# Optimization experiments

Hardware: AMD Instinct MI355X
Metric: run time of the kernel (lower is better)

Reference implementation:

```python
import jax, jax.numpy as jnp
import numpy as np

B, T, D, H, E, K = 1, 2048, 768, 12, 8, 2
VOCAB, LLOC, LGLOB, CHUNK = 32000, 2, 1, 16
D4 = 4 * D


def setup_inputs() -> dict:
    key = jax.random.key(0)
    kit = iter(jax.random.split(key, 40))

    def rn(shape, scale=0.02):
        return jax.random.normal(next(kit), shape, jnp.float32) * scale

    d = {
        "x_emb": jax.random.normal(next(kit), (B, T, D), jnp.float32),
        "latent_code": jax.random.normal(next(kit), (B, D), jnp.float32),
        "pos_emb": rn((T, D)),
    }
    for pfx, L in (("loc", LLOC), ("glob", LGLOB)):
        d[pfx + "_ln1_s"] = jnp.ones((L, D), jnp.float32)
        d[pfx + "_ln1_b"] = jnp.zeros((L, D), jnp.float32)
        d[pfx + "_ln2_s"] = jnp.ones((L, D), jnp.float32)
        d[pfx + "_ln2_b"] = jnp.zeros((L, D), jnp.float32)
        d[pfx + "_attn_w"] = rn((L, 3 * D, D))
        d[pfx + "_attn_b"] = jnp.zeros((L, 3 * D), jnp.float32)
        d[pfx + "_out_w"] = rn((L, D, D))
        d[pfx + "_out_b"] = jnp.zeros((L, D), jnp.float32)
        d[pfx + "_router_w"] = rn((L, E, D))
        d[pfx + "_w1"] = rn((L, E, D4, D))
        d[pfx + "_b1"] = jnp.zeros((L, E, D4), jnp.float32)
        d[pfx + "_w2"] = rn((L, E, D, D4))
        d[pfx + "_b2"] = jnp.zeros((L, E, D), jnp.float32)
    d["glob_lat_router_w"] = rn((LGLOB, E, D))
    d["ln_s"] = jnp.ones((D,), jnp.float32)
    d["ln_b"] = jnp.zeros((D,), jnp.float32)
    d["head_w"] = rn((VOCAB, D))
    return d


def _ln(x, s, b):
    m = x.mean(-1, keepdims=True)
    v = ((x - m) ** 2).mean(-1, keepdims=True)
    return (x - m) / jnp.sqrt(v + 1e-5) * s + b


def _mha(x, wqkv, bqkv, wo, bo, mask):
    b_, t_, d_ = x.shape
    hd = d_ // H
    q, k, v = jnp.split(x @ wqkv.T + bqkv, 3, axis=-1)
    q = q.reshape(b_, t_, H, hd)
    k = k.reshape(b_, t_, H, hd)
    v = v.reshape(b_, t_, H, hd)
    sc = jnp.einsum('bqhd,bkhd->bhqk', q, k) / jnp.sqrt(jnp.float32(hd))
    sc = jnp.where(mask, -jnp.inf, sc)
    a = jax.nn.softmax(sc, axis=-1)
    o = jnp.einsum('bhqk,bkhd->bqhd', a, v).reshape(b_, t_, d_)
    return o @ wo.T + bo


def _moe(x, rw, w1, b1, w2, b2, lat_logits):
    # top-k routed MoE: combine weight is exactly 0 for unselected experts,
    # so dense per-expert compute weighted by we reproduces the gather/scatter math.
    b_, t_, d_ = x.shape
    xf = x.reshape(-1, d_)
    logits = xf @ rw.T  # [N,E]
    if lat_logits is not None:
        logits = (logits.reshape(b_, t_, E) + lat_logits[:, None, :]).reshape(-1, E)
    probs = jax.nn.softmax(logits, axis=-1)
    w, sel = jax.lax.top_k(probs, K)
    w = w / w.sum(-1, keepdims=True)
    onehot = (sel[..., None] == jnp.arange(E)).astype(xf.dtype)  # [N,K,E]
    we = (w[..., None] * onehot).sum(1)  # [N,E]
    out = jnp.zeros_like(xf)
    for e in range(E):
        h = jax.nn.gelu(xf @ w1[e].T + b1[e], approximate=False)
        out = out + we[:, e:e + 1] * (h @ w2[e].T + b2[e])
    bal = E * jnp.sum(probs.mean(0) * onehot.max(1).mean(0))
    return out.reshape(b_, t_, d_), bal


def _run_layers(x, mask, lat_code, ln1_s, ln1_b, ln2_s, ln2_b, aw, ab, ow, ob, rw, lrw, w1, b1, w2, b2):
    bal = jnp.float32(0.0)
    for l in range(ln1_s.shape[0]):
        h = _ln(x, ln1_s[l], ln1_b[l])
        x = x + _mha(h, aw[l], ab[l], ow[l], ob[l], mask)
        h = _ln(x, ln2_s[l], ln2_b[l])
        lat_logits = None if lat_code is None else lat_code @ lrw[l].T
        mo, b = _moe(h, rw[l], w1[l], b1[l], w2[l], b2[l], lat_logits)
        x = x + mo
        bal = bal + b
    return x, bal


def reference(x_emb, latent_code, pos_emb,
              loc_ln1_s, loc_ln1_b, loc_ln2_s, loc_ln2_b, loc_attn_w, loc_attn_b, loc_out_w, loc_out_b,
              loc_router_w, loc_w1, loc_b1, loc_w2, loc_b2,
              glob_ln1_s, glob_ln1_b, glob_ln2_s, glob_ln2_b, glob_attn_w, glob_attn_b, glob_out_w, glob_out_b,
              glob_router_w, glob_w1, glob_b1, glob_w2, glob_b2, glob_lat_router_w,
              ln_s, ln_b, head_w):
    b_, t_, d_ = x_emb.shape
    x = x_emb + pos_emb[:t_][None]
    mask = jnp.triu(jnp.ones((t_, t_), bool), 1)
    h_local, bal_l = _run_layers(x, mask, None, loc_ln1_s, loc_ln1_b, loc_ln2_s, loc_ln2_b,
                                 loc_attn_w, loc_attn_b, loc_out_w, loc_out_b,
                                 loc_router_w, None, loc_w1, loc_b1, loc_w2, loc_b2)
    # T divisible by CHUNK, so synopsis idxs are 15,31,...,T-1 (no extra append)
    syn = h_local[:, CHUNK - 1::CHUNK]  # [B,S,D]
    gin = jnp.concatenate([latent_code[:, None, :], syn], axis=1)  # [B,S+1,D]
    s1 = gin.shape[1]
    gmask = jnp.triu(jnp.ones((s1, s1), bool), 1)
    h_g, bal_g = _run_layers(gin, gmask, latent_code, glob_ln1_s, glob_ln1_b, glob_ln2_s, glob_ln2_b,
                             glob_attn_w, glob_attn_b, glob_out_w, glob_out_b,
                             glob_router_w, glob_lat_router_w, glob_w1, glob_b1, glob_w2, glob_b2)
    gc = h_g[:, :-1]  # [B,S,D] (latent prepended -> drop last)
    # uniform chunks: broadcast each chunk's global context over its 16 tokens
    out = (h_local.reshape(b_, t_ // CHUNK, CHUNK, d_) + gc[:, :, None, :]).reshape(b_, t_, d_)
    out = _ln(out, ln_s, ln_b)
    return out @ head_w.T, bal_l + bal_g
```

## Files before the change

### kernel.cpp

```cpp
#include <hip/hip_runtime.h>

constexpr int TT   = 2048;
constexpr int DD   = 768;
constexpr int NH   = 12;
constexpr int NE   = 8;
constexpr int DFF  = 3072;
constexpr int NV   = 32000;
constexpr int S1R  = 129;
constexpr int QKVLD = 3 * DD;

constexpr int BM = 64, BN = 64, BK = 16;

__device__ __forceinline__ float gelu_f(float v) {
  return 0.5f * v * (1.0f + erff(v * 0.70710678118654752f));
}

__global__ void add_pos_kernel(const float* __restrict__ xe, const float* __restrict__ pe,
                               float* __restrict__ X, int n) {
  int i = blockIdx.x * blockDim.x + threadIdx.x;
  if (i < n) X[i] = xe[i] + pe[i];
}

__global__ void zero_i32(int* p, int n) {
  int i = blockIdx.x * blockDim.x + threadIdx.x;
  if (i < n) p[i] = 0;
}
__global__ void zero_f32(float* p, int n) {
  int i = blockIdx.x * blockDim.x + threadIdx.x;
  if (i < n) p[i] = 0.f;
}

__global__ __launch_bounds__(256)
void ln_kernel(const float* __restrict__ Xin, const float* __restrict__ s,
               const float* __restrict__ b, float* __restrict__ Y, int rows) {
  int t = blockIdx.x;
  if (t >= rows) return;
  const float* xr = Xin + (size_t)t * DD;
  int tid = threadIdx.x;
  float x0 = xr[tid], x1 = xr[tid + 256], x2 = xr[tid + 512];
  __shared__ float red[256];
  red[tid] = x0 + x1 + x2;
  __syncthreads();
  for (int k = 128; k > 0; k >>= 1) { if (tid < k) red[tid] += red[tid + k]; __syncthreads(); }
  float mean = red[0] * (1.f / 768.f);
  __syncthreads();
  float d0 = x0 - mean, d1 = x1 - mean, d2 = x2 - mean;
  red[tid] = d0 * d0 + d1 * d1 + d2 * d2;
  __syncthreads();
  for (int k = 128; k > 0; k >>= 1) { if (tid < k) red[tid] += red[tid + k]; __syncthreads(); }
  float inv = 1.f / sqrtf(red[0] * (1.f / 768.f) + 1e-5f);
  float* yr = Y + (size_t)t * DD;
  yr[tid]       = d0 * inv * s[tid]       + b[tid];
  yr[tid + 256] = d1 * inv * s[tid + 256] + b[tid + 256];
  yr[tid + 512] = d2 * inv * s[tid + 512] + b[tid + 512];
}

template <bool ADD_C>
__global__ __launch_bounds__(256)
void gemm_tn(const float* __restrict__ A, const float* __restrict__ W,
             const float* __restrict__ bias, float* __restrict__ C,
             int M, int N, int Kd) {
  __shared__ float As[BK][BM + 4];
  __shared__ float Ws[BK][BN + 4];
  int n0 = blockIdx.x * BN, m0 = blockIdx.y * BM;
  int tid = threadIdx.x;
  int tx = tid & 15, ty = tid >> 4;
  int lrow = tid >> 2, lk4 = (tid & 3) * 4;
  float acc[4][4] = {};
  for (int k0 = 0; k0 < Kd; k0 += BK) {
    {
      int r = m0 + lrow;
      float4 v = (r < M) ? *(const float4*)(A + (size_t)r * Kd + k0 + lk4)
                         : make_float4(0.f, 0.f, 0.f, 0.f);
      As[lk4 + 0][lrow] = v.x; As[lk4 + 1][lrow] = v.y;
      As[lk4 + 2][lrow] = v.z; As[lk4 + 3][lrow] = v.w;
    }
    {
      int r = n0 + lrow;
      float4 v = (r < N) ? *(const float4*)(W + (size_t)r * Kd + k0 + lk4)
                         : make_float4(0.f, 0.f, 0.f, 0.f);
      Ws[lk4 + 0][lrow] = v.x; Ws[lk4 + 1][lrow] = v.y;
      Ws[lk4 + 2][lrow] = v.z; Ws[lk4 + 3][lrow] = v.w;
    }
    __syncthreads();
#pragma unroll
    for (int k = 0; k < BK; k++) {
      float a[4], b[4];
#pragma unroll
      for (int i = 0; i < 4; i++) a[i] = As[k][ty * 4 + i];
#pragma unroll
      for (int j = 0; j < 4; j++) b[j] = Ws[k][tx * 4 + j];
#pragma unroll
      for (int i = 0; i < 4; i++)
#pragma unroll
        for (int j = 0; j < 4; j++) acc[i][j] = fmaf(a[i], b[j], acc[i][j]);
    }
    __syncthreads();
  }
#pragma unroll
  for (int i = 0; i < 4; i++) {
    int r = m0 + ty * 4 + i;
    if (r >= M) continue;
#pragma unroll
    for (int j = 0; j < 4; j++) {
      int c = n0 + tx * 4 + j;
      if (c >= N) continue;
      float v = acc[i][j] + (bias ? bias[c] : 0.f);
      size_t idx = (size_t)r * N + c;
      if (ADD_C) C[idx] += v; else C[idx] = v;
    }
  }
}

__global__ __launch_bounds__(256)
void moe_gemm1(const float* __restrict__ Xin, const float* __restrict__ W1,
               const float* __restrict__ B1, float* __restrict__ H1,
               const int* __restrict__ perm, const int* __restrict__ off) {
  __shared__ float As[BK][BM + 4];
  __shared__ float Ws[BK][BN + 4];
  int e = blockIdx.z;
  int mstart = off[e];
  int mcnt = off[e + 1] - mstart;
  int m0 = blockIdx.y * BM;
  if (m0 >= mcnt) return;
  int n0 = blockIdx.x * BN;
  const float* W = W1 + (size_t)e * DFF * DD;
  const float* bias = B1 + (size_t)e * DFF;
  int tid = threadIdx.x;
  int tx = tid & 15, ty = tid >> 4;
  int lrow = tid >> 2, lk4 = (tid & 3) * 4;
  int gm = m0 + lrow;
  const float* arow = (gm < mcnt) ? (Xin + (size_t)perm[mstart + gm] * DD) : nullptr;
  float acc[4][4] = {};
  for (int k0 = 0; k0 < DD; k0 += BK) {
    float4 va = arow ? *(const float4*)(arow + k0 + lk4) : make_float4(0.f, 0.f, 0.f, 0.f);
    As[lk4 + 0][lrow] = va.x; As[lk4 + 1][lrow] = va.y;
    As[lk4 + 2][lrow] = va.z; As[lk4 + 3][lrow] = va.w;
    int wr = n0 + lrow;
    float4 vw = *(const float4*)(W + (size_t)wr * DD + k0 + lk4);
    Ws[lk4 + 0][lrow] = vw.x; Ws[lk4 + 1][lrow] = vw.y;
    Ws[lk4 + 2][lrow] = vw.z; Ws[lk4 + 3][lrow] = vw.w;
    __syncthreads();
#pragma unroll
    for (int k = 0; k < BK; k++) {
      float a[4], b[4];
#pragma unroll
      for (int i = 0; i < 4; i++) a[i] = As[k][ty * 4 + i];
#pragma unroll
      for (int j = 0; j < 4; j++) b[j] = Ws[k][tx * 4 + j];
#pragma unroll
      for (int i = 0; i < 4; i++)
#pragma unroll
        for (int j = 0; j < 4; j++) acc[i][j] = fmaf(a[i], b[j], acc[i][j]);
    }
    __syncthreads();
  }
#pragma unroll
  for (int i = 0; i < 4; i++) {
    int r = m0 + ty * 4 + i;
    if (r >= mcnt) continue;
#pragma unroll
    for (int j = 0; j < 4; j++) {
      int c = n0 + tx * 4 + j;
      float v = acc[i][j] + bias[c];
      H1[(size_t)(mstart + r) * DFF + c] = gelu_f(v);
    }
  }
}

__global__ __launch_bounds__(256)
void moe_gemm2(const float* __restrict__ H1, const float* __restrict__ W2,
               const float* __restrict__ B2, float* __restrict__ Xout,
               const int* __restrict__ perm, const int* __restrict__ off,
               const float* __restrict__ wlist) {
  __shared__ float As[BK][BM + 4];
  __shared__ float Ws[BK][BN + 4];
  int e = blockIdx.z;
  int mstart = off[e];
  int mcnt = off[e + 1] - mstart;
  int m0 = blockIdx.y * BM;
  if (m0 >= mcnt) return;
  int n0 = blockIdx.x * BN;
  const float* W = W2 + (size_t)e * DD * DFF;
  const float* bias = B2 + (size_t)e * DD;
  int tid = threadIdx.x;
  int tx = tid & 15, ty = tid >> 4;
  int lrow = tid >> 2, lk4 = (tid & 3) * 4;
  int gm = m0 + lrow;
  const float* arow = (gm < mcnt) ? (H1 + (size_t)(mstart + gm) * DFF) : nullptr;
  float acc[4][4] = {};
  for (int k0 = 0; k0 < DFF; k0 += BK) {
    float4 va = arow ? *(const float4*)(arow + k0 + lk4) : make_float4(0.f, 0.f, 0.f, 0.f);
    As[lk4 + 0][lrow] = va.x; As[lk4 + 1][lrow] = va.y;
    As[lk4 + 2][lrow] = va.z; As[lk4 + 3][lrow] = va.w;
    int wr = n0 + lrow;
    float4 vw = *(const float4*)(W + (size_t)wr * DFF + k0 + lk4);
    Ws[lk4 + 0][lrow] = vw.x; Ws[lk4 + 1][lrow] = vw.y;
    Ws[lk4 + 2][lrow] = vw.z; Ws[lk4 + 3][lrow] = vw.w;
    __syncthreads();
#pragma unroll
    for (int k = 0; k < BK; k++) {
      float a[4], b[4];
#pragma unroll
      for (int i = 0; i < 4; i++) a[i] = As[k][ty * 4 + i];
#pragma unroll
      for (int j = 0; j < 4; j++) b[j] = Ws[k][tx * 4 + j];
#pragma unroll
      for (int i = 0; i < 4; i++)
#pragma unroll
        for (int j = 0; j < 4; j++) acc[i][j] = fmaf(a[i], b[j], acc[i][j]);
    }
    __syncthreads();
  }
#pragma unroll
  for (int i = 0; i < 4; i++) {
    int r = m0 + ty * 4 + i;
    if (r >= mcnt) continue;
    int tok = perm[mstart + r];
    float sc = wlist[mstart + r];
#pragma unroll
    for (int j = 0; j < 4; j++) {
      int c = n0 + tx * 4 + j;
      float v = (acc[i][j] + bias[c]) * sc;
      atomicAdd(&Xout[(size_t)tok * DD + c], v);
    }
  }
}

__global__ __launch_bounds__(64)
void attn_kernel(const float* __restrict__ QKV, float* __restrict__ O, int Tlen) {
  int q = blockIdx.x, h = blockIdx.y;
  int tid = threadIdx.x;
  __shared__ float qv[64];
  __shared__ float sc[TT];
  qv[tid] = QKV[(size_t)q * QKVLD + h * 64 + tid];
  __syncthreads();
  int nk = q + 1;
  for (int k = tid; k < nk; k += 64) {
    const float* kr = QKV + (size_t)k * QKVLD + DD + h * 64;
    float s = 0.f;
#pragma unroll
    for (int d = 0; d < 64; d++) s = fmaf(qv[d], kr[d], s);
    sc[k] = s * 0.125f;
  }
  __syncthreads();
  float m = -1e30f;
  for (int k = tid; k < nk; k += 64) m = fmaxf(m, sc[k]);
#pragma unroll
  for (int o = 32; o > 0; o >>= 1) m = fmaxf(m, __shfl_down(m, o));
  m = __shfl(m, 0);
  float ssum = 0.f;
  for (int k = tid; k < nk; k += 64) {
    float e = __expf(sc[k] - m);
    sc[k] = e;
    ssum += e;
  }
#pragma unroll
  for (int o = 32; o > 0; o >>= 1) ssum += __shfl_down(ssum, o);
  ssum = __shfl(ssum, 0);
  float inv = 1.f / ssum;
  __syncthreads();
  float acc = 0.f;
  const float* vbase = QKV + 2 * DD + h * 64 + tid;
  for (int k = 0; k < nk; k++) acc = fmaf(sc[k], vbase[(size_t)k * QKVLD], acc);
  O[(size_t)q * DD + h * 64 + tid] = acc * inv;
}

__global__ __launch_bounds__(64)
void router_kernel(const float* __restrict__ Hin, const float* __restrict__ RW,
                   const float* __restrict__ latent, const float* __restrict__ LRW,
                   int rows, int* __restrict__ selbuf, float* __restrict__ wbuf,
                   float* __restrict__ probbuf, int* __restrict__ cnt) {
  int t = blockIdx.x;
  if (t >= rows) return;
  int tid = threadIdx.x;
  const float* hr = Hin + (size_t)t * DD;
  __shared__ float logit[NE];
  for (int e = 0; e < NE; e++) {
    const float* w = RW + (size_t)e * DD;
    float p = 0.f;
    for (int d = tid; d < DD; d += 64) p = fmaf(hr[d], w[d], p);
    if (LRW) {
      const float* lw = LRW + (size_t)e * DD;
      for (int d = tid; d < DD; d += 64) p = fmaf(latent[d], lw[d], p);
    }
#pragma unroll
    for (int o = 32; o > 0; o >>= 1) p += __shfl_down(p, o);
    if (tid == 0) logit[e] = p;
  }
  __syncthreads();
  if (tid == 0) {
    float mx = logit[0];
    for (int e = 1; e < NE; e++) mx = fmaxf(mx, logit[e]);
    float pe[NE], ssum = 0.f;
    for (int e = 0; e < NE; e++) { pe[e] = __expf(logit[e] - mx); ssum += pe[e]; }
    float inv = 1.f / ssum;
    for (int e = 0; e < NE; e++) { pe[e] *= inv; probbuf[(size_t)t * NE + e] = pe[e]; }
    int e0 = 0;
    for (int e = 1; e < NE; e++) if (pe[e] > pe[e0]) e0 = e;
    int e1 = -1;
    for (int e = 0; e < NE; e++) {
      if (e == e0) continue;
      if (e1 < 0 || pe[e] > pe[e1]) e1 = e;
    }
    float wsum = pe[e0] + pe[e1];
    selbuf[t * 2] = e0; selbuf[t * 2 + 1] = e1;
    wbuf[t * 2] = pe[e0] / wsum; wbuf[t * 2 + 1] = pe[e1] / wsum;
    atomicAdd(&cnt[e0], 1);
    atomicAdd(&cnt[e1], 1);
  }
}

__global__ __launch_bounds__(256)
void prob_reduce(const float* __restrict__ probbuf, float* __restrict__ prob_sum, int rows) {
  int e = blockIdx.x, tid = threadIdx.x;
  float s = 0.f;
  for (int t = tid; t < rows; t += 256) s += probbuf[(size_t)t * NE + e];
  __shared__ float red[256];
  red[tid] = s;
  __syncthreads();
  for (int k = 128; k > 0; k >>= 1) { if (tid < k) red[tid] += red[tid + k]; __syncthreads(); }
  if (tid == 0) prob_sum[e] = red[0];
}

__global__ void scan_bal(const int* __restrict__ cnt, int* __restrict__ off,
                         int* __restrict__ fill, const float* __restrict__ prob_sum,
                         float* __restrict__ bal, int rows) {
  if (threadIdx.x == 0 && blockIdx.x == 0) {
    int acc = 0;
    for (int e = 0; e < NE; e++) { off[e] = acc; acc += cnt[e]; fill[e] = 0; }
    off[NE] = acc;
    float invr = 1.f / (float)rows;
    float b = 0.f;
    for (int e = 0; e < NE; e++) b += (prob_sum[e] * invr) * ((float)cnt[e] * invr);
    bal[0] += (float)NE * b;
  }
}

__global__ void fill_kernel(const int* __restrict__ selbuf, const float* __restrict__ wbuf,
                            const int* __restrict__ off, int* __restrict__ fill,
                            int* __restrict__ perm, float* __restrict__ wlist, int rows) {
  int t = blockIdx.x * blockDim.x + threadIdx.x;
  if (t >= rows) return;
  for (int k = 0; k < 2; k++) {
    int e = selbuf[t * 2 + k];
    int pos = atomicAdd(&fill[e], 1);
    perm[off[e] + pos] = t;
    wlist[off[e] + pos] = wbuf[t * 2 + k];
  }
}

__global__ void build_gin(const float* __restrict__ X, const float* __restrict__ latent,
                          float* __restrict__ G) {
  int i = blockIdx.x * blockDim.x + threadIdx.x;
  if (i >= S1R * DD) return;
  int r = i / DD, d = i - r * DD;
  G[i] = (r == 0) ? latent[d] : X[(size_t)((r - 1) * 16 + 15) * DD + d];
}

__global__ void compose_kernel(const float* __restrict__ X, const float* __restrict__ G,
                               float* __restrict__ F) {
  int i = blockIdx.x * blockDim.x + threadIdx.x;
  if (i >= TT * DD) return;
  int t = i / DD, d = i - t * DD;
  F[i] = X[i] + G[(size_t)(t >> 4) * DD + d];
}

__global__ void write_bal(const float* __restrict__ bal, float* __restrict__ out) {
  if (threadIdx.x == 0 && blockIdx.x == 0) out[(size_t)TT * NV] = bal[0];
}

extern "C" void kernel_launch(void* const* d_in, const int* in_sizes, int n_in,
                              void* d_out, int out_size, void* d_ws, size_t ws_size,
                              hipStream_t stream) {
  (void)in_sizes; (void)n_in; (void)out_size; (void)ws_size;
  const float* x_emb    = (const float*)d_in[0];
  const float* latent   = (const float*)d_in[1];
  const float* pos_emb  = (const float*)d_in[2];
  const float* loc_ln1_s = (const float*)d_in[3];
  const float* loc_ln1_b = (const float*)d_in[4];
  const float* loc_ln2_s = (const float*)d_in[5];
  const float* loc_ln2_b = (const float*)d_in[6];
  const float* loc_aw    = (const float*)d_in[7];
  const float* loc_ab    = (const float*)d_in[8];
  const float* loc_ow    = (const float*)d_in[9];
  const float* loc_ob    = (const float*)d_in[10];
  const float* loc_rw    = (const float*)d_in[11];
  const float* loc_w1    = (const float*)d_in[12];
  const float* loc_b1    = (const float*)d_in[13];
  const float* loc_w2    = (const float*)d_in[14];
  const float* loc_b2    = (const float*)d_in[15];
  const float* glb_ln1_s = (const float*)d_in[16];
  const float* glb_ln1_b = (const float*)d_in[17];
  const float* glb_ln2_s = (const float*)d_in[18];
  const float* glb_ln2_b = (const float*)d_in[19];
  const float* glb_aw    = (const float*)d_in[20];
  const float* glb_ab    = (const float*)d_in[21];
  const float* glb_ow    = (const float*)d_in[22];
  const float* glb_ob    = (const float*)d_in[23];
  const float* glb_rw    = (const float*)d_in[24];
  const float* glb_w1    = (const float*)d_in[25];
  const float* glb_b1    = (const float*)d_in[26];
  const float* glb_w2    = (const float*)d_in[27];
  const float* glb_b2    = (const float*)d_in[28];
  const float* glb_lrw   = (const float*)d_in[29];
  const float* ln_s      = (const float*)d_in[30];
  const float* ln_b      = (const float*)d_in[31];
  const float* head_w    = (const float*)d_in[32];
  float* out = (float*)d_out;

  float* base = (float*)d_ws;
  float* X    = base;
  float* Hb   = X    + (size_t)TT * DD;
  float* QKV  = Hb   + (size_t)TT * DD;
  float* ATTO = QKV  + (size_t)TT * QKVLD;
  float* H1   = ATTO + (size_t)TT * DD;
  float* G    = H1   + (size_t)4096 * DFF;
  float* PROB = G    + (size_t)S1R * DD;
  float* WL   = PROB + (size_t)TT * NE;
  float* WB   = WL   + 4096;
  float* PS   = WB   + (size_t)TT * 2;
  float* BAL  = PS   + 16;
  int*   SEL  = (int*)(BAL + 16);
  int*   PERM = SEL  + 2 * TT;
  int*   CNT  = PERM + 4096;
  int*   FILL = CNT  + 16;
  int*   OFFP = FILL + 16;

  auto run_layer = [&](float* Xp, int rows,
                       const float* l1s, const float* l1b,
                       const float* l2s, const float* l2b,
                       const float* aw, const float* ab,
                       const float* ow, const float* ob,
                       const float* rw, const float* w1, const float* b1,
                       const float* w2, const float* b2,
                       const float* lat, const float* lrw) {
    int mg = (rows + BM - 1) / BM;
    ln_kernel<<<rows, 256, 0, stream>>>(Xp, l1s, l1b, Hb, rows);
    gemm_tn<false><<<dim3(QKVLD / BN, mg), 256, 0, stream>>>(Hb, aw, ab, QKV, rows, QKVLD, DD);
    attn_kernel<<<dim3(rows, NH), 64, 0, stream>>>(QKV, ATTO, rows);
    gemm_tn<true><<<dim3(DD / BN, mg), 256, 0, stream>>>(ATTO, ow, ob, Xp, rows, DD, DD);
    ln_kernel<<<rows, 256, 0, stream>>>(Xp, l2s, l2b, Hb, rows);
    zero_i32<<<1, 32, 0, stream>>>(CNT, 16);
    router_kernel<<<rows, 64, 0, stream>>>(Hb, rw, lat, lrw, rows, SEL, WB, PROB, CNT);
    prob_reduce<<<NE, 256, 0, stream>>>(PROB, PS, rows);
    scan_bal<<<1, 64, 0, stream>>>(CNT, OFFP, FILL, PS, BAL, rows);
    fill_kernel<<<(rows + 255) / 256, 256, 0, stream>>>(SEL, WB, OFFP, FILL, PERM, WL, rows);
    moe_gemm1<<<dim3(DFF / BN, mg, NE), 256, 0, stream>>>(Hb, w1, b1, H1, PERM, OFFP);
    moe_gemm2<<<dim3(DD / BN, mg, NE), 256, 0, stream>>>(H1, w2, b2, Xp, PERM, OFFP, WL);
  };

  add_pos_kernel<<<(TT * DD + 255) / 256, 256, 0, stream>>>(x_emb, pos_emb, X, TT * DD);
  zero_f32<<<1, 32, 0, stream>>>(BAL, 1);

  for (int l = 0; l < 2; l++) {
    run_layer(X, TT,
              loc_ln1_s + (size_t)l * DD, loc_ln1_b + (size_t)l * DD,
              loc_ln2_s + (size_t)l * DD, loc_ln2_b + (size_t)l * DD,
              loc_aw + (size_t)l * QKVLD * DD, loc_ab + (size_t)l * QKVLD,
              loc_ow + (size_t)l * DD * DD, loc_ob + (size_t)l * DD,
              loc_rw + (size_t)l * NE * DD,
              loc_w1 + (size_t)l * NE * DFF * DD, loc_b1 + (size_t)l * NE * DFF,
              loc_w2 + (size_t)l * NE * DD * DFF, loc_b2 + (size_t)l * NE * DD,
              nullptr, nullptr);
  }

  build_gin<<<(S1R * DD + 255) / 256, 256, 0, stream>>>(X, latent, G);
  run_layer(G, S1R,
            glb_ln1_s, glb_ln1_b, glb_ln2_s, glb_ln2_b,
            glb_aw, glb_ab, glb_ow, glb_ob,
            glb_rw, glb_w1, glb_b1, glb_w2, glb_b2,
            latent, glb_lrw);

  float* Fbuf = QKV;
  float* FN   = ATTO;
  compose_kernel<<<(TT * DD + 255) / 256, 256, 0, stream>>>(X, G, Fbuf);
  ln_kernel<<<TT, 256, 0, stream>>>(Fbuf, ln_s, ln_b, FN, TT);
  gemm_tn<false><<<dim3(NV / BN, TT / BM), 256, 0, stream>>>(FN, head_w, nullptr, out, TT, NV, DD);
  write_bal<<<1, 1, 0, stream>>>(BAL, out);
}
```

Before: 6.844 ms.

## Run vocab head GEMM on bf16 MFMA with async LDS loads

Replaces the fp32 scalar-FMA tiled GEMM for the 2048x32000x768 vocabulary projection with a bf16 MFMA kernel. It uses 128x128 tiles, direct global-to-LDS loads and an XOR-swizzled shared layout. The activations and the head weights are cast to bf16 on every call, reusing the Hb and H1 scratch buffers. This cuts the compute cost of the largest GEMM, at the price of reduced precision in the logits and extra cast passes over the 98 MB head weight.

```diff
diff --git a/kernel.cpp b/kernel.cpp
--- a/kernel.cpp
+++ b/kernel.cpp
@@ -11,8 +11,23 @@
 
 constexpr int BM = 64, BN = 64, BK = 16;
 
+typedef __attribute__((ext_vector_type(8))) short bf16x8;
+typedef __attribute__((ext_vector_type(4))) float f32x4;
+
 __device__ __forceinline__ float gelu_f(float v) {
   return 0.5f * v * (1.0f + erff(v * 0.70710678118654752f));
+}
+
+__device__ __forceinline__ ushort f2bf(float f) {
+  unsigned u = __float_as_uint(f);
+  u = (u + 0x7fffu + ((u >> 16) & 1u)) >> 16;
+  return (ushort)u;
+}
+
+__device__ __forceinline__ void gload_lds16(const void* g, void* l) {
+  __builtin_amdgcn_global_load_lds(
+      (const __attribute__((address_space(1))) unsigned int*)g,
+      (__attribute__((address_space(3))) unsigned int*)l, 16, 0, 0);
 }
 
 __global__ void add_pos_kernel(const float* __restrict__ xe, const float* __restrict__ pe,
@@ -28,6 +43,16 @@
 __global__ void zero_f32(float* p, int n) {
   int i = blockIdx.x * blockDim.x + threadIdx.x;
   if (i < n) p[i] = 0.f;
+}
+
+__global__ __launch_bounds__(256)
+void cast_bf16_kernel(const float* __restrict__ in, ushort* __restrict__ out, int n) {
+  int i = (blockIdx.x * blockDim.x + threadIdx.x) * 4;
+  if (i >= n) return;
+  float4 v = *(const float4*)(in + i);
+  ushort4 o;
+  o.x = f2bf(v.x); o.y = f2bf(v.y); o.z = f2bf(v.z); o.w = f2bf(v.w);
+  *(ushort4*)(out + i) = o;
 }
 
 __global__ __launch_bounds__(256)
@@ -108,6 +133,70 @@
       float v = acc[i][j] + (bias ? bias[c] : 0.f);
       size_t idx = (size_t)r * N + c;
       if (ADD_C) C[idx] += v; else C[idx] = v;
+    }
+  }
+}
+
+__global__ __launch_bounds__(256)
+void head_gemm_bf16(const ushort* __restrict__ A, const ushort* __restrict__ W,
+                    float* __restrict__ C, int M, int N, int K) {
+  __shared__ ushort As[128 * 64];
+  __shared__ ushort Bs[128 * 64];
+  int tid  = threadIdx.x;
+  int lane = tid & 63, wid = tid >> 6;
+  int wm = wid >> 1, wn = wid & 1;
+  int m0 = blockIdx.y * 128, n0 = blockIdx.x * 128;
+
+  f32x4 acc[4][4] = {};
+
+  int rl = lane & 15, cs = lane >> 4;
+
+  for (int k0 = 0; k0 < K; k0 += 64) {
+#pragma unroll
+    for (int r = 0; r < 4; ++r) {
+      int chunk = (r * 4 + wid) << 10;
+      int o     = chunk + lane * 16;
+      int row   = o >> 7;
+      int slot  = ((o >> 4) & 7) ^ (row & 7);
+      gload_lds16(A + (size_t)(m0 + row) * K + k0 + slot * 8, (char*)As + chunk);
+      gload_lds16(W + (size_t)(n0 + row) * K + k0 + slot * 8, (char*)Bs + chunk);
+    }
+    __syncthreads();
+
+    bf16x8 af[4][2], bfr[4][2];
+#pragma unroll
+    for (int mi = 0; mi < 4; ++mi) {
+      int m = wm * 64 + mi * 16 + rl;
+      int n = wn * 64 + mi * 16 + rl;
+#pragma unroll
+      for (int ks = 0; ks < 2; ++ks) {
+        int sa = (ks * 4 + cs) ^ (m & 7);
+        int sb = (ks * 4 + cs) ^ (n & 7);
+        af[mi][ks]  = *(const bf16x8*)((const char*)As + m * 128 + sa * 16);
+        bfr[mi][ks] = *(const bf16x8*)((const char*)Bs + n * 128 + sb * 16);
+      }
+    }
+#pragma unroll
+    for (int mi = 0; mi < 4; ++mi)
+#pragma unroll
+      for (int ni = 0; ni < 4; ++ni)
+#pragma unroll
+        for (int ks = 0; ks < 2; ++ks)
+          acc[mi][ni] = __builtin_amdgcn_mfma_f32_16x16x32_bf16(
+              af[mi][ks], bfr[ni][ks], acc[mi][ni], 0, 0, 0);
+    __syncthreads();
+  }
+
+#pragma unroll
+  for (int mi = 0; mi < 4; ++mi) {
+    int row = m0 + wm * 64 + mi * 16 + cs * 4;
+#pragma unroll
+    for (int ni = 0; ni < 4; ++ni) {
+      int col = n0 + wn * 64 + ni * 16 + rl;
+      f32x4 v = acc[mi][ni];
+#pragma unroll
+      for (int r = 0; r < 4; ++r)
+        C[(size_t)(row + r) * N + col] = v[r];
     }
   }
 }
@@ -476,6 +565,12 @@
   float* FN   = ATTO;
   compose_kernel<<<(TT * DD + 255) / 256, 256, 0, stream>>>(X, G, Fbuf);
   ln_kernel<<<TT, 256, 0, stream>>>(Fbuf, ln_s, ln_b, FN, TT);
-  gemm_tn<false><<<dim3(NV / BN, TT / BM), 256, 0, stream>>>(FN, head_w, nullptr, out, TT, NV, DD);
+
+  ushort* Abf = (ushort*)Hb;
+  ushort* Wbf = (ushort*)H1;
+  cast_bf16_kernel<<<(TT * DD / 4 + 255) / 256, 256, 0, stream>>>(FN, Abf, TT * DD);
+  cast_bf16_kernel<<<(NV * DD / 4 + 255) / 256, 256, 0, stream>>>(head_w, Wbf, NV * DD);
+  head_gemm_bf16<<<dim3(NV / 128, TT / 128), 256, 0, stream>>>(Abf, Wbf, out, TT, NV, DD);
+
   write_bal<<<1, 1, 0, stream>>>(BAL, out);
 }
```

Result: faster. 5.554 ms (-18.9%).
